# Kernel optimization log

Measured on AMD Instinct MI355X. Metric: run time of the kernel, lower is better.

Reference implementation:

```python
import math
import jax, jax.numpy as jnp
import numpy as np

N_HEADS = 16
N_KV_HEADS = 4
HEAD_DIM = 64
DIM = 1024
WINDOW = 16
EPS = 0.01


def _alibi_slopes(n_heads):
    closest = 2 ** math.floor(math.log2(n_heads))
    base = 2.0 ** (-2.0 ** (-(math.log2(closest) - 3)))
    slopes = base ** np.arange(1, closest + 1, dtype=np.float32)
    if closest < n_heads:
        eb = 2.0 ** (-2.0 ** (-(math.log2(2 * closest) - 3)))
        extra = eb ** np.arange(1, 2 * (n_heads - closest) + 1, 2, dtype=np.float32)
        slopes = np.concatenate([slopes, extra])
    return jnp.asarray(slopes[:n_heads])


def _rmsnorm(x, w):
    xf = x.astype(jnp.float32)
    norm = jax.lax.rsqrt(jnp.mean(xf * xf, axis=-1, keepdims=True) + EPS)
    return (xf * norm).astype(x.dtype) * w


def setup_inputs() -> dict:
    key = jax.random.key(0)
    ks = jax.random.split(key, 6)
    B, L = 2, 2048
    s = 1.0 / math.sqrt(DIM)
    return {
        "x": jax.random.normal(ks[0], (B, L, DIM), jnp.float32),
        "wq": jax.random.normal(ks[1], (N_HEADS * HEAD_DIM, DIM), jnp.float32) * s,
        "wk": jax.random.normal(ks[2], (N_KV_HEADS * HEAD_DIM, DIM), jnp.float32) * s,
        "wv": jax.random.normal(ks[3], (N_KV_HEADS * HEAD_DIM, DIM), jnp.float32) * s,
        "wo": jax.random.normal(ks[4], (DIM, N_HEADS * HEAD_DIM), jnp.float32) * s,
        "q_norm_w": jnp.ones((HEAD_DIM,), jnp.float32),
        "k_norm_w": jnp.ones((HEAD_DIM,), jnp.float32),
    }


def reference(x, wq, wk, wv, wo, q_norm_w, k_norm_w):
    B, L, _ = x.shape
    n_rep = N_HEADS // N_KV_HEADS
    q = (x @ wq.T).reshape(B, L, N_HEADS, HEAD_DIM)
    k = (x @ wk.T).reshape(B, L, N_KV_HEADS, HEAD_DIM)
    v = (x @ wv.T).reshape(B, L, N_KV_HEADS, HEAD_DIM)
    q = _rmsnorm(q, q_norm_w)
    k = _rmsnorm(k, k_norm_w)
    # GQA repeat: head h maps to kv head (h % n_kv_heads), matching torch expand order
    k = jnp.broadcast_to(k[:, :, None], (B, L, n_rep, N_KV_HEADS, HEAD_DIM)).reshape(B, L, N_HEADS, HEAD_DIM)
    v = jnp.broadcast_to(v[:, :, None], (B, L, n_rep, N_KV_HEADS, HEAD_DIM)).reshape(B, L, N_HEADS, HEAD_DIM)
    # ALiBi bias with causal + sliding-window mask
    pos = jnp.arange(L)
    rel = pos[None, :] - pos[:, None]  # [L, L], j - i
    slopes = _alibi_slopes(N_HEADS)  # [H]
    bias = slopes[:, None, None] * rel[None].astype(jnp.float32)  # [H, L, L]
    masked = (rel > 0) | (rel < -WINDOW)
    bias = jnp.where(masked[None], -jnp.inf, bias)
    scale = 1.0 / math.sqrt(HEAD_DIM)
    attn = jnp.einsum("bqhd,bkhd->bhqk", q, k) * scale + bias[None]
    attn = jax.nn.softmax(attn, axis=-1)
    out = jnp.einsum("bhqk,bkhd->bqhd", attn, v).reshape(B, L, N_HEADS * HEAD_DIM)
    return out @ wo.T
```

## Files before the change

### kernel.cpp

```cpp
#include <hip/hip_runtime.h>
#include <math.h>

#define DIM 1024
#define NH 16
#define NKV 4
#define HD 64
#define WINDOW 16
#define EPS 0.01f

typedef __bf16 bf16_t;
typedef bf16_t bf16x8 __attribute__((ext_vector_type(8)));
typedef bf16_t bf16x4 __attribute__((ext_vector_type(4)));
typedef float f32x4 __attribute__((ext_vector_type(4)));

__global__ __launch_bounds__(256) void f2bf_all(const float* __restrict__ x,
                                                const float* __restrict__ wq,
                                                const float* __restrict__ wk,
                                                const float* __restrict__ wv,
                                                const float* __restrict__ wo,
                                                bf16_t* __restrict__ xb,
                                                bf16_t* __restrict__ wqkvb,
                                                bf16_t* __restrict__ wob) {
  int i = blockIdx.x * blockDim.x + threadIdx.x;
  const float* src;
  bf16_t* dst;
  int off;
  if (i < 1048576) { src = x; dst = xb; off = i; }
  else if (i < 1310720) { src = wq; dst = wqkvb; off = i - 1048576; }
  else if (i < 1376256) { src = wk; dst = wqkvb + (size_t)1024 * DIM; off = i - 1310720; }
  else if (i < 1441792) { src = wv; dst = wqkvb + (size_t)1280 * DIM; off = i - 1376256; }
  else { src = wo; dst = wob; off = i - 1441792; }
  float4 f = ((const float4*)src)[off];
  bf16x4 o = {(bf16_t)f.x, (bf16_t)f.y, (bf16_t)f.z, (bf16_t)f.w};
  ((bf16x4*)dst)[off] = o;
}


#define GEMM_STAGE(buf, Ag, Bg)                                                 \
  {                                                                             \
    _Pragma("unroll")                                                           \
    for (int it = 0; it < 4; it++) {                                            \
      int c = it * 256 + t;                                                     \
      int r = c >> 3;                                                           \
      int kc = ((c & 7) - r) & 7;                                               \
      __builtin_amdgcn_global_load_lds(                                         \
          (const __attribute__((address_space(1))) void*)((Ag) + (size_t)r * K + kc * 8), \
          (__attribute__((address_space(3))) void*)(As[buf] + c * 8), 16, 0, 0); \
    }                                                                           \
    _Pragma("unroll")                                                           \
    for (int it = 0; it < 2; it++) {                                            \
      int c = it * 256 + t;                                                     \
      int r = c >> 3;                                                           \
      int kc = ((c & 7) - r) & 7;                                               \
      __builtin_amdgcn_global_load_lds(                                         \
          (const __attribute__((address_space(1))) void*)((Bg) + (size_t)r * K + kc * 8), \
          (__attribute__((address_space(3))) void*)(Bs[buf] + c * 8), 16, 0, 0); \
    }                                                                           \
  }

#define GEMM_DBUF_LOOP(Aptr, Bptr)                                              \
  {                                                                             \
    const bf16_t* Abase = Aptr + (size_t)row0 * K;                              \
    const bf16_t* Bbase = Bptr + (size_t)col0 * K;                              \
    GEMM_STAGE(0, Abase, Bbase)                                                 \
    const int nIter = K >> 6;                                                   \
    for (int ki = 0; ki < nIter; ki++) {                                        \
      __syncthreads();                                                          \
      if (ki + 1 < nIter)                                                       \
        GEMM_STAGE((ki + 1) & 1, Abase + (ki + 1) * 64, Bbase + (ki + 1) * 64)  \
      const bf16_t* Ab = As[ki & 1];                                            \
      const bf16_t* Bb = Bs[ki & 1];                                            \
      _Pragma("unroll")                                                         \
      for (int h = 0; h < 2; h++) {                                             \
        bf16x8 af[2], bfr[4];                                                   \
        _Pragma("unroll")                                                       \
        for (int mi = 0; mi < 2; mi++) af[mi] = *(const bf16x8*)(Ab + aoff[h][mi]); \
        _Pragma("unroll")                                                       \
        for (int ni = 0; ni < 4; ni++) bfr[ni] = *(const bf16x8*)(Bb + boff[h][ni]); \
        _Pragma("unroll")                                                       \
        for (int mi = 0; mi < 2; mi++)                                          \
          _Pragma("unroll")                                                     \
          for (int ni = 0; ni < 4; ni++)                                        \
            acc[mi][ni] = __builtin_amdgcn_mfma_f32_16x16x32_bf16(af[mi], bfr[ni], \
                                                                  acc[mi][ni], 0, 0, 0); \
      }                                                                         \
    }                                                                           \
  }

#define GEMM_PROLOGUE(NBX, BYX)                                                 \
  const int t = threadIdx.x;                                                    \
  const int lane = t & 63;                                                      \
  const int wid = t >> 6;                                                       \
  const int xcd = blockIdx.x & 7;                                               \
  const int jj = blockIdx.x >> 3;                                               \
  const int bx = jj % (NBX);                                                    \
  const int row0 = (xcd * (BYX) + jj / (NBX)) * 128;                            \
  const int col0 = bx * 64;                                                     \
  const int wm = wid * 32;                                                      \
  const int lquad = lane >> 4;                                                  \
  const int lcol = lane & 15;                                                   \
  int aoff[2][2], boff[2][4];                                                   \
  _Pragma("unroll")                                                             \
  for (int h = 0; h < 2; h++) {                                                 \
    _Pragma("unroll")                                                           \
    for (int mi = 0; mi < 2; mi++) {                                            \
      int r = wm + mi * 16 + lcol;                                              \
      aoff[h][mi] = r * 64 + (((h * 4 + lquad) + r) & 7) * 8;                   \
    }                                                                           \
    _Pragma("unroll")                                                           \
    for (int ni = 0; ni < 4; ni++) {                                            \
      int r = ni * 16 + lcol;                                                   \
      boff[h][ni] = r * 64 + (((h * 4 + lquad) + r) & 7) * 8;                   \
    }                                                                           \
  }                                                                             \
  f32x4 acc[2][4] = {};

__global__ __launch_bounds__(256) void gemm_qkv_rms(const bf16_t* __restrict__ A,
                                                    const bf16_t* __restrict__ B,
                                                    bf16_t* __restrict__ C,
                                                    const float* __restrict__ qw,
                                                    const float* __restrict__ kw,
                                                    int M, int N, int K) {
  __shared__ bf16_t As[2][128 * 64];
  __shared__ bf16_t Bs[2][64 * 64];
  GEMM_PROLOGUE(24, 4)
  GEMM_DBUF_LOOP(A, B)

  const int hcol = bx;
  const bool isv = (hcol >= 20);
  float wreg[4];
  if (!isv) {
    const float* wp = (hcol < 16) ? qw : kw;
#pragma unroll
    for (int ni = 0; ni < 4; ni++) wreg[ni] = wp[ni * 16 + lcol];
  }

#pragma unroll
  for (int mi = 0; mi < 2; mi++) {
#pragma unroll
    for (int r = 0; r < 4; r++) {
      float norm = 1.0f;
      if (!isv) {
        float ss = 0.0f;
#pragma unroll
        for (int ni = 0; ni < 4; ni++) ss += acc[mi][ni][r] * acc[mi][ni][r];
#pragma unroll
        for (int off = 8; off >= 1; off >>= 1) ss += __shfl_xor(ss, off);
        norm = rsqrtf(ss * (1.0f / 64.0f) + EPS);
      }
      size_t base = (size_t)(row0 + wm + mi * 16 + lquad * 4 + r) * N + col0 + lcol;
#pragma unroll
      for (int ni = 0; ni < 4; ni++) {
        float v = acc[mi][ni][r] * norm;
        if (!isv) v *= wreg[ni];
        C[base + ni * 16] = (bf16_t)v;
      }
    }
  }
}

template <typename CT, int NBX, int BYX>
__global__ __launch_bounds__(256) void gemm_bf16(const bf16_t* __restrict__ A,
                                                 const bf16_t* __restrict__ B,
                                                 CT* __restrict__ C,
                                                 int M, int N, int K) {
  __shared__ bf16_t As[2][128 * 64];
  __shared__ bf16_t Bs[2][64 * 64];
  GEMM_PROLOGUE(NBX, BYX)
  GEMM_DBUF_LOOP(A, B)

#pragma unroll
  for (int mi = 0; mi < 2; mi++)
#pragma unroll
    for (int ni = 0; ni < 4; ni++) {
      size_t base = (size_t)(row0 + wm + mi * 16 + lquad * 4) * N + col0 + ni * 16 + lcol;
#pragma unroll
      for (int r = 0; r < 4; r++)
        C[base + (size_t)r * N] = (CT)acc[mi][ni][r];
    }
}

#define LKP 72
#define LVP 40

__global__ __launch_bounds__(1024) void attn_mfma(const bf16_t* __restrict__ qkv,
                                                  bf16_t* __restrict__ y) {
  __shared__ bf16_t Ks[4][32][LKP];
  __shared__ bf16_t VTs[4][64][LVP];
  __shared__ bf16_t Ps[16][16][LVP];

  const int t = threadIdx.x;
  const int lane = t & 63;
  const int w = t >> 6;
  const int b = blockIdx.x >> 7;
  const int i0loc = (blockIdx.x & 127) << 4;
  const int rowbase = b << 11;
  const int rowg0 = rowbase + i0loc;

  {
    int kvh = t >> 8;
    int key = (t >> 3) & 31;
    int dc = t & 7;
    int jloc = i0loc - 16 + key;
    int rg = rowbase + (jloc < 0 ? 0 : jloc);
    const bf16_t* src = qkv + (size_t)rg * 1536 + 1024 + kvh * 64 + dc * 8;
    bf16x8 kval = *(const bf16x8*)src;
    *(bf16x8*)(&Ks[kvh][key][dc * 8]) = kval;
    bf16x8 vval = *(const bf16x8*)(src + 256);
    int kslot = ((key >> 3) ^ (dc & 3)) * 8 + (key & 7);
#pragma unroll
    for (int e = 0; e < 8; e++) VTs[kvh][dc * 8 + e][kslot] = vval[e];
  }
  __syncthreads();

  const int col = lane & 15;
  const int quad = lane >> 4;
  const int h = w;
  const int kvh = w & 3;
  const float slope = exp2f(-0.5f * (float)(h + 1));

  bf16x8 kf[2][2];
#pragma unroll
  for (int kt = 0; kt < 2; kt++)
#pragma unroll
    for (int kc = 0; kc < 2; kc++)
      kf[kt][kc] = *(const bf16x8*)(&Ks[kvh][kt * 16 + col][kc * 32 + quad * 8]);
  bf16x8 vf[4];
#pragma unroll
  for (int nt = 0; nt < 4; nt++) {
    int dim = nt * 16 + col;
    int kchunk = quad ^ ((dim >> 3) & 3);
    vf[nt] = *(const bf16x8*)(&VTs[kvh][dim][kchunk * 8]);
  }

  const bf16_t* qrow = qkv + (size_t)(rowg0 + col) * 1536 + h * 64;
  bf16x8 qf0 = *(const bf16x8*)(qrow + quad * 8);
  bf16x8 qf1 = *(const bf16x8*)(qrow + 32 + quad * 8);

  f32x4 s0 = {}, s1 = {};
  s0 = __builtin_amdgcn_mfma_f32_16x16x32_bf16(qf0, kf[0][0], s0, 0, 0, 0);
  s0 = __builtin_amdgcn_mfma_f32_16x16x32_bf16(qf1, kf[0][1], s0, 0, 0, 0);
  s1 = __builtin_amdgcn_mfma_f32_16x16x32_bf16(qf0, kf[1][0], s1, 0, 0, 0);
  s1 = __builtin_amdgcn_mfma_f32_16x16x32_bf16(qf1, kf[1][1], s1, 0, 0, 0);

  const bool t0dead = (i0loc == 0);
  float sc0[4], sc1[4];
#pragma unroll
  for (int r = 0; r < 4; r++) {
    int rel0 = col - 16 - (quad * 4 + r);
    int rel1 = rel0 + 16;
    bool m0 = t0dead || (rel0 < -WINDOW);
    bool m1 = (rel1 > 0);
    sc0[r] = m0 ? -INFINITY : s0[r] * 0.125f + slope * (float)rel0;
    sc1[r] = m1 ? -INFINITY : s1[r] * 0.125f + slope * (float)rel1;
  }
  float mx[4], sum[4], p0[4], p1[4];
#pragma unroll
  for (int r = 0; r < 4; r++) mx[r] = fmaxf(sc0[r], sc1[r]);
#pragma unroll
  for (int off = 8; off >= 1; off >>= 1)
#pragma unroll
    for (int r = 0; r < 4; r++) mx[r] = fmaxf(mx[r], __shfl_xor(mx[r], off));
#pragma unroll
  for (int r = 0; r < 4; r++) {
    p0[r] = __expf(sc0[r] - mx[r]);
    p1[r] = __expf(sc1[r] - mx[r]);
    sum[r] = p0[r] + p1[r];
  }
#pragma unroll
  for (int off = 8; off >= 1; off >>= 1)
#pragma unroll
    for (int r = 0; r < 4; r++) sum[r] += __shfl_xor(sum[r], off);

#pragma unroll
  for (int r = 0; r < 4; r++) {
    Ps[w][quad * 4 + r][col] = (bf16_t)p0[r];
    Ps[w][quad * 4 + r][16 + col] = (bf16_t)p1[r];
  }
  bf16x8 pf = *(const bf16x8*)(&Ps[w][col][quad * 8]);

  f32x4 o[4] = {};
#pragma unroll
  for (int nt = 0; nt < 4; nt++)
    o[nt] = __builtin_amdgcn_mfma_f32_16x16x32_bf16(pf, vf[nt], o[nt], 0, 0, 0);

#pragma unroll
  for (int nt = 0; nt < 4; nt++)
#pragma unroll
    for (int r = 0; r < 4; r++)
      y[(size_t)(rowg0 + quad * 4 + r) * 1024 + h * 64 + nt * 16 + col] =
          (bf16_t)(o[nt][r] / sum[r]);
}

extern "C" void kernel_launch(void* const* d_in, const int* in_sizes, int n_in,
                              void* d_out, int out_size, void* d_ws, size_t ws_size,
                              hipStream_t stream) {
  const float* x  = (const float*)d_in[0];
  const float* wq = (const float*)d_in[1];
  const float* wk = (const float*)d_in[2];
  const float* wv = (const float*)d_in[3];
  const float* wo = (const float*)d_in[4];
  const float* qw = (const float*)d_in[5];
  const float* kw = (const float*)d_in[6];
  float* out = (float*)d_out;

  const int M = 4096;

  bf16_t* xb    = (bf16_t*)d_ws;
  bf16_t* wqkvb = xb + (size_t)M * DIM;
  bf16_t* wob   = wqkvb + (size_t)1536 * DIM;
  bf16_t* qkv   = wob + (size_t)DIM * DIM;
  bf16_t* yb    = qkv + (size_t)M * 1536;

  dim3 blk(256);
  f2bf_all<<<1703936 / 256, blk, 0, stream>>>(x, wq, wk, wv, wo, xb, wqkvb, wob);

  gemm_qkv_rms<<<768, blk, 0, stream>>>(xb, wqkvb, qkv, qw, kw, M, 1536, DIM);

  attn_mfma<<<256, dim3(1024), 0, stream>>>(qkv, yb);

  gemm_bf16<float, 16, 4><<<512, blk, 0, stream>>>(yb, wob, out, M, DIM, DIM);
}
```

Measured before the change: 126.7 us.

## Load GEMM B fragments directly into registers instead of staging through LDS

The B (weight) tile no longer goes through shared memory. Each lane reads its bf16x8 MFMA fragments straight from global memory into registers and prefetches them one K-step ahead, while A stays double-buffered in LDS. This removes the LDS traffic and space for B and lowers LDS pressure. In exchange, all four waves reload the same B fragments from global/L2, each read is a 16-byte strided access, register use rises, and a second __syncthreads is added per iteration.

```diff
diff --git a/kernel.cpp b/kernel.cpp
--- a/kernel.cpp
+++ b/kernel.cpp
@@ -36,7 +36,7 @@
 }
 
 
-#define GEMM_STAGE(buf, Ag, Bg)                                                 \
+#define GEMM_STAGE_A(buf, Ag)                                                   \
   {                                                                             \
     _Pragma("unroll")                                                           \
     for (int it = 0; it < 4; it++) {                                            \
@@ -47,43 +47,49 @@
           (const __attribute__((address_space(1))) void*)((Ag) + (size_t)r * K + kc * 8), \
           (__attribute__((address_space(3))) void*)(As[buf] + c * 8), 16, 0, 0); \
     }                                                                           \
+  }
+
+#define LOAD_BFR(dst, kbase)                                                    \
+  {                                                                             \
     _Pragma("unroll")                                                           \
-    for (int it = 0; it < 2; it++) {                                            \
-      int c = it * 256 + t;                                                     \
-      int r = c >> 3;                                                           \
-      int kc = ((c & 7) - r) & 7;                                               \
-      __builtin_amdgcn_global_load_lds(                                         \
-          (const __attribute__((address_space(1))) void*)((Bg) + (size_t)r * K + kc * 8), \
-          (__attribute__((address_space(3))) void*)(Bs[buf] + c * 8), 16, 0, 0); \
-    }                                                                           \
+    for (int h = 0; h < 2; h++)                                                 \
+      _Pragma("unroll")                                                         \
+      for (int ni = 0; ni < 4; ni++)                                            \
+        dst[h][ni] = *(const bf16x8*)(Bfrag0 + (size_t)ni * 16 * K + (h * 32) + (kbase)); \
   }
 
 #define GEMM_DBUF_LOOP(Aptr, Bptr)                                              \
+  const bf16_t* Abase = Aptr + (size_t)row0 * K;                                \
+  const bf16_t* Bfrag0 = Bptr + (size_t)(col0 + lcol) * K + lquad * 8;          \
+  bf16x8 bfrC[2][4], bfrN[2][4];                                                \
+  GEMM_STAGE_A(0, Abase)                                                        \
+  LOAD_BFR(bfrN, 0)                                                             \
   {                                                                             \
-    const bf16_t* Abase = Aptr + (size_t)row0 * K;                              \
-    const bf16_t* Bbase = Bptr + (size_t)col0 * K;                              \
-    GEMM_STAGE(0, Abase, Bbase)                                                 \
     const int nIter = K >> 6;                                                   \
     for (int ki = 0; ki < nIter; ki++) {                                        \
       __syncthreads();                                                          \
-      if (ki + 1 < nIter)                                                       \
-        GEMM_STAGE((ki + 1) & 1, Abase + (ki + 1) * 64, Bbase + (ki + 1) * 64)  \
+      if (ki + 1 < nIter) {                                                     \
+        GEMM_STAGE_A((ki + 1) & 1, Abase + (ki + 1) * 64)                       \
+      }                                                                         \
+      _Pragma("unroll")                                                         \
+      for (int h = 0; h < 2; h++)                                               \
+        _Pragma("unroll")                                                       \
+        for (int ni = 0; ni < 4; ni++) bfrC[h][ni] = bfrN[h][ni];               \
+      if (ki + 1 < nIter) LOAD_BFR(bfrN, (ki + 1) * 64)                         \
       const bf16_t* Ab = As[ki & 1];                                            \
-      const bf16_t* Bb = Bs[ki & 1];                                            \
       _Pragma("unroll")                                                         \
       for (int h = 0; h < 2; h++) {                                             \
-        bf16x8 af[2], bfr[4];                                                   \
+        bf16x8 af[2];                                                           \
         _Pragma("unroll")                                                       \
         for (int mi = 0; mi < 2; mi++) af[mi] = *(const bf16x8*)(Ab + aoff[h][mi]); \
-        _Pragma("unroll")                                                       \
-        for (int ni = 0; ni < 4; ni++) bfr[ni] = *(const bf16x8*)(Bb + boff[h][ni]); \
         _Pragma("unroll")                                                       \
         for (int mi = 0; mi < 2; mi++)                                          \
           _Pragma("unroll")                                                     \
           for (int ni = 0; ni < 4; ni++)                                        \
-            acc[mi][ni] = __builtin_amdgcn_mfma_f32_16x16x32_bf16(af[mi], bfr[ni], \
+            acc[mi][ni] = __builtin_amdgcn_mfma_f32_16x16x32_bf16(af[mi], bfrC[h][ni], \
                                                                   acc[mi][ni], 0, 0, 0); \
       }                                                                         \
+      __syncthreads();                                                          \
     }                                                                           \
   }
 
@@ -99,7 +105,7 @@
   const int wm = wid * 32;                                                      \
   const int lquad = lane >> 4;                                                  \
   const int lcol = lane & 15;                                                   \
-  int aoff[2][2], boff[2][4];                                                   \
+  int aoff[2][2];                                                               \
   _Pragma("unroll")                                                             \
   for (int h = 0; h < 2; h++) {                                                 \
     _Pragma("unroll")                                                           \
@@ -107,11 +113,6 @@
       int r = wm + mi * 16 + lcol;                                              \
       aoff[h][mi] = r * 64 + (((h * 4 + lquad) + r) & 7) * 8;                   \
     }                                                                           \
-    _Pragma("unroll")                                                           \
-    for (int ni = 0; ni < 4; ni++) {                                            \
-      int r = ni * 16 + lcol;                                                   \
-      boff[h][ni] = r * 64 + (((h * 4 + lquad) + r) & 7) * 8;                   \
-    }                                                                           \
   }                                                                             \
   f32x4 acc[2][4] = {};
 
@@ -122,7 +123,6 @@
                                                     const float* __restrict__ kw,
                                                     int M, int N, int K) {
   __shared__ bf16_t As[2][128 * 64];
-  __shared__ bf16_t Bs[2][64 * 64];
   GEMM_PROLOGUE(24, 4)
   GEMM_DBUF_LOOP(A, B)
 
@@ -165,7 +165,6 @@
                                                  CT* __restrict__ C,
                                                  int M, int N, int K) {
   __shared__ bf16_t As[2][128 * 64];
-  __shared__ bf16_t Bs[2][64 * 64];
   GEMM_PROLOGUE(NBX, BYX)
   GEMM_DBUF_LOOP(A, B)
 
```

New measurement: 182.1 us. +43.7%, slower.
